# Kernel tuning notes

Measured on AMD Instinct MI355X. Metric: run time of the kernel, lower is better.

## Reference

```python
import jax, jax.numpy as jnp
import numpy as np

D_MODEL = 1024
H = 16
D_K = D_MODEL // H
NEG = -1.0e9


def setup_inputs() -> dict:
    key = jax.random.key(0)
    ks = jax.random.split(key, 12)
    B, S = 2, 2048
    s = 1.0 / np.sqrt(D_MODEL)
    inp = {
        "q": jax.random.normal(ks[0], (B, S, D_MODEL), jnp.float32),
        "k": jax.random.normal(ks[1], (B, S, D_MODEL), jnp.float32),
        "v": jax.random.normal(ks[2], (B, S, D_MODEL), jnp.float32),
        "mask": jnp.tril(jnp.ones((S, S), jnp.int32))[None, None, :, :],
        "wq": jax.random.normal(ks[3], (D_MODEL, D_MODEL), jnp.float32) * s,
        "bq": jax.random.normal(ks[4], (D_MODEL,), jnp.float32) * s,
        "wk": jax.random.normal(ks[5], (D_MODEL, D_MODEL), jnp.float32) * s,
        "bk": jax.random.normal(ks[6], (D_MODEL,), jnp.float32) * s,
        "wv": jax.random.normal(ks[7], (D_MODEL, D_MODEL), jnp.float32) * s,
        "bv": jax.random.normal(ks[8], (D_MODEL,), jnp.float32) * s,
        "wo": jax.random.normal(ks[9], (D_MODEL, D_MODEL), jnp.float32) * s,
        "bo": jax.random.normal(ks[10], (D_MODEL,), jnp.float32) * s,
    }
    return inp


def _split_heads(x):
    # [B,S,D] -> [B,H,S,d_k]
    B, S, _ = x.shape
    return x.reshape(B, S, H, D_K).transpose(0, 2, 1, 3)


def reference(q, k, v, mask, wq, bq, wk, bk, wv, bv, wo, bo):
    # torch Linear: y = x @ W.T + b
    query = _split_heads(q @ wq.T + bq)
    key = _split_heads(k @ wk.T + bk)
    value = _split_heads(v @ wv.T + bv)
    # scores: [B,H,S,S]
    scores = jnp.einsum("bhqd,bhkd->bhqk", query, key) / jnp.sqrt(
        jnp.asarray(D_K, query.dtype))
    scores = jnp.where(mask == 0, jnp.asarray(NEG, scores.dtype), scores)
    attn = jax.nn.softmax(scores, axis=-1)  # dropout p=0.0 -> identity
    x = jnp.einsum("bhqk,bhkd->bhqd", attn, value)
    B, _, S, _ = x.shape
    x = x.transpose(0, 2, 1, 3).reshape(B, S, D_MODEL)
    return x @ wo.T + bo
```

## Files before the change

kernel.cpp:

```cpp
#include <hip/hip_runtime.h>
#include <hip/hip_bf16.h>
#include <cstdint>
#include <cstddef>

#define BATCH 2
#define SEQ   2048
#define DM    1024
#define NH    16
#define DK    64
#define MROWS (BATCH*SEQ)

typedef __bf16 bf16;
typedef float  f32x4  __attribute__((ext_vector_type(4)));
typedef bf16   bf16x8 __attribute__((ext_vector_type(8)));
typedef bf16   bf16x4 __attribute__((ext_vector_type(4)));

#define MFMA32(a, b, c) __builtin_amdgcn_mfma_f32_16x16x32_bf16(a, b, c, 0, 0, 0)

__device__ __forceinline__ void llds16(const void* gc, void* l) {
    void* g = (void*)gc;
    __builtin_amdgcn_global_load_lds(
        (__attribute__((address_space(1))) uint32_t*)g,
        (__attribute__((address_space(3))) uint32_t*)l,
        16, 0, 0);
}

__global__ __launch_bounds__(256) void k_convert(
    const float* __restrict__ q, const float* __restrict__ k, const float* __restrict__ v,
    const float* __restrict__ wq, const float* __restrict__ wk, const float* __restrict__ wv,
    const float* __restrict__ wo,
    bf16* __restrict__ qb, bf16* __restrict__ kb, bf16* __restrict__ vb,
    bf16* __restrict__ wqb, bf16* __restrict__ wkb, bf16* __restrict__ wvb,
    bf16* __restrict__ wob) {
    long t = (long)blockIdx.x * blockDim.x + threadIdx.x;
    const long NQ = (long)MROWS * DM / 4;
    const long NW = (long)DM * DM / 4;
    const float* src; bf16* dst; long off;
    if (t < NQ)            { src = q;  dst = qb;  off = t; }
    else if (t < 2*NQ)     { src = k;  dst = kb;  off = t - NQ; }
    else if (t < 3*NQ)     { src = v;  dst = vb;  off = t - 2*NQ; }
    else {
        long u = t - 3*NQ;
        if (u < NW)        { src = wq; dst = wqb; off = u; }
        else if (u < 2*NW) { src = wk; dst = wkb; off = u - NW; }
        else if (u < 3*NW) { src = wv; dst = wvb; off = u - 2*NW; }
        else               { src = wo; dst = wob; off = u - 3*NW; }
    }
    f32x4 x = *(const f32x4*)(src + off * 4);
    bf16x4 y;
    y[0] = (bf16)x[0]; y[1] = (bf16)x[1]; y[2] = (bf16)x[2]; y[3] = (bf16)x[3];
    *(bf16x4*)(dst + off * 4) = y;
}

__device__ __forceinline__ void gemm_main(const bf16* __restrict__ A, const bf16* __restrict__ B,
                                          int m0, int n0, f32x4 acc[4][4]) {
    constexpr int K = DM, BK = 64;
    __shared__ bf16 sA[16 * 512];
    __shared__ bf16 sB[16 * 512];
    const int tid = threadIdx.x;
    const int l = tid & 63, w = tid >> 6;
    const int lr = l & 15, lc = l >> 4;
    const int wm = w & 1, wn = w >> 1;

    for (int k0 = 0; k0 < K; k0 += BK) {
#pragma unroll
        for (int i = 0; i < 4; ++i) {
            int e = w * 4 + i;
            int kc = e >> 3, t16 = e & 7;
            const bf16* ga = A + (size_t)(m0 + t16 * 16 + lr) * K + k0 + kc * 32 + lc * 8;
            const bf16* gb = B + (size_t)(n0 + t16 * 16 + lr) * K + k0 + kc * 32 + lc * 8;
            llds16(ga, &sA[e * 512]);
            llds16(gb, &sB[e * 512]);
        }
        __syncthreads();

#pragma unroll
        for (int kk = 0; kk < 2; ++kk) {
            bf16x8 af[4], bfr[4];
#pragma unroll
            for (int mi = 0; mi < 4; ++mi)
                af[mi] = *(const bf16x8*)&sA[(size_t)(kk * 8 + wm * 4 + mi) * 512 + l * 8];
#pragma unroll
            for (int ni = 0; ni < 4; ++ni)
                bfr[ni] = *(const bf16x8*)&sB[(size_t)(kk * 8 + wn * 4 + ni) * 512 + l * 8];
#pragma unroll
            for (int mi = 0; mi < 4; ++mi)
#pragma unroll
                for (int ni = 0; ni < 4; ++ni)
                    acc[mi][ni] = MFMA32(af[mi], bfr[ni], acc[mi][ni]);
        }
        __syncthreads();
    }
}

__global__ __launch_bounds__(256) void k_gemm_qkv(
    const bf16* __restrict__ qb, const bf16* __restrict__ kb, const bf16* __restrict__ vb,
    const bf16* __restrict__ wqb, const bf16* __restrict__ wkb, const bf16* __restrict__ wvb,
    const float* __restrict__ bq, const float* __restrict__ bk, const float* __restrict__ bv,
    bf16* __restrict__ Qf, bf16* __restrict__ Kf, bf16* __restrict__ Vf) {
    const int z = blockIdx.z;
    const bf16* A; const bf16* B; const float* bias;
    int m0, n0;
    if (z == 2) {
        A = vb; B = wvb; bias = bv;
        m0 = blockIdx.x * 128;
        n0 = blockIdx.y * 128;
    } else {
        A = z ? wkb : wqb; B = z ? kb : qb; bias = z ? bk : bq;
        m0 = blockIdx.y * 128;
        n0 = blockIdx.x * 128;
    }
    f32x4 acc[4][4] = {};
    gemm_main(A, B, m0, n0, acc);

    const int tid = threadIdx.x, l = tid & 63, w = tid >> 6;
    const int quad = l >> 4, l15 = l & 15;
    const int wm = w & 1, wn = w >> 1;

    if (z == 2) {
#pragma unroll
        for (int ni = 0; ni < 4; ++ni) {
            int dcol = n0 + wn * 64 + ni * 16 + l15;
            int hh2 = dcol >> 6;
            int dtile = (dcol >> 4) & 3;
            float bias_v = bias[dcol];
#pragma unroll
            for (int mi = 0; mi < 4; ++mi) {
                int srow = m0 + wm * 64 + mi * 16;
                int bb = srow >> 11, sl = srow & 2047;
                int kc = sl >> 5;
                int qp = 2 * (mi & 1) + (quad >> 1);
                bf16x4 pack;
#pragma unroll
                for (int r = 0; r < 4; ++r)
                    pack[r] = (bf16)(acc[mi][ni][r] + bias_v);
                size_t entry = ((size_t)(bb * NH + hh2) * 64 + kc) * 4 + dtile;
                *(bf16x4*)(Vf + entry * 512 + (size_t)(qp * 16 + l15) * 8 + (quad & 1) * 4) = pack;
            }
        }
    } else {
        bf16* out = z ? Kf : Qf;
        const float scale = z ? 1.0f : 0.18033688f;
        float bias_rv[4][4];
#pragma unroll
        for (int mi = 0; mi < 4; ++mi)
#pragma unroll
            for (int r = 0; r < 4; ++r)
                bias_rv[mi][r] = bias[m0 + wm * 64 + mi * 16 + quad * 4 + r];
#pragma unroll
        for (int ni = 0; ni < 4; ++ni) {
            int scol = n0 + wn * 64 + ni * 16 + l15;
            int bb = scol >> 11, s = scol & 2047;
            int s16 = s >> 4;
#pragma unroll
            for (int mi = 0; mi < 4; ++mi) {
                int drow = m0 + wm * 64 + mi * 16;
                int hh2 = (drow >> 6) & 15;
                int chunk = (drow & 63) >> 5;
                int qp = 2 * (mi & 1) + (quad >> 1);
                bf16x4 pack;
#pragma unroll
                for (int r = 0; r < 4; ++r)
                    pack[r] = (bf16)((acc[mi][ni][r] + bias_rv[mi][r]) * scale);
                size_t entry = ((size_t)(bb * NH + hh2) * 128 + s16) * 2 + chunk;
                *(bf16x4*)(out + entry * 512 + (size_t)(qp * 16 + l15) * 8 + (quad & 1) * 4) = pack;
            }
        }
    }
}

__global__ __launch_bounds__(256) void k_gemm_out(
    const bf16* __restrict__ X, const bf16* __restrict__ wob,
    const float* __restrict__ bo, float* __restrict__ out) {
    constexpr int K = DM, BK = 64;
    const int m0 = blockIdx.y * 128, n0 = blockIdx.x * 64;
    __shared__ bf16 sA[16 * 512];
    __shared__ bf16 sB[8 * 512];
    const int tid = threadIdx.x;
    const int l = tid & 63, w = tid >> 6;
    const int lr = l & 15, lc = l >> 4;
    const int quad = l >> 4, l15 = l & 15;
    const int wm = w & 1, wn = w >> 1;

    f32x4 acc[4][2] = {};
    for (int k0 = 0; k0 < K; k0 += BK) {
#pragma unroll
        for (int i = 0; i < 4; ++i) {
            int e = w * 4 + i;
            int kc = e >> 3, mt = e & 7;
            llds16(X + (size_t)(m0 + mt * 16 + lr) * K + k0 + kc * 32 + lc * 8, &sA[e * 512]);
        }
#pragma unroll
        for (int i = 0; i < 2; ++i) {
            int e = w * 2 + i;
            int kc = e >> 2, nt = e & 3;
            llds16(wob + (size_t)(n0 + nt * 16 + lr) * K + k0 + kc * 32 + lc * 8, &sB[e * 512]);
        }
        __syncthreads();

#pragma unroll
        for (int kk = 0; kk < 2; ++kk) {
            bf16x8 af[4], bfr[2];
#pragma unroll
            for (int mi = 0; mi < 4; ++mi)
                af[mi] = *(const bf16x8*)&sA[(size_t)(kk * 8 + wm * 4 + mi) * 512 + l * 8];
#pragma unroll
            for (int ni = 0; ni < 2; ++ni)
                bfr[ni] = *(const bf16x8*)&sB[(size_t)(kk * 4 + wn * 2 + ni) * 512 + l * 8];
#pragma unroll
            for (int mi = 0; mi < 4; ++mi)
#pragma unroll
                for (int ni = 0; ni < 2; ++ni)
                    acc[mi][ni] = MFMA32(af[mi], bfr[ni], acc[mi][ni]);
        }
        __syncthreads();
    }
#pragma unroll
    for (int mi = 0; mi < 4; ++mi)
#pragma unroll
        for (int ni = 0; ni < 2; ++ni) {
            int col = n0 + wn * 32 + ni * 16 + l15;
            float bias_v = bo[col];
            int rbase = m0 + wm * 64 + mi * 16 + quad * 4;
#pragma unroll
            for (int r = 0; r < 4; ++r)
                out[(size_t)(rbase + r) * DM + col] = acc[mi][ni][r] + bias_v;
        }
}

__global__ __launch_bounds__(256, 4) void k_flash(const bf16* __restrict__ Qf,
                                                  const bf16* __restrict__ Kf,
                                                  const bf16* __restrict__ Vf,
                                                  bf16* __restrict__ X) {
    const int bh = blockIdx.x;
    const int qt = 31 - (int)blockIdx.y;
    const int b = bh >> 4, h = bh & 15;
    const int tid = threadIdx.x, w = tid >> 6, l = tid & 63;
    const int quad = l >> 4, l15 = l & 15;
    __shared__ bf16 sK[8 * 512];
    __shared__ bf16 sV[8 * 512];
    __shared__ bf16 P[4][16 * 72];
    bf16* Pw = P[w];

    const bf16* qfp = Qf + (size_t)bh * 128 * 1024;
    const bf16* kfp = Kf + (size_t)bh * 128 * 1024;
    const bf16* vfp = Vf + (size_t)bh * 64 * 4 * 512;

    const int qt16 = qt * 4 + w;
    const int qglob = qt16 * 16 + l15;

    bf16x8 qf[2];
#pragma unroll
    for (int c = 0; c < 2; ++c)
        qf[c] = *(const bf16x8*)(qfp + ((size_t)qt16 * 2 + c) * 512 + (size_t)l * 8);

    f32x4 o[4] = {};
    float lp = 0.f;

    for (int j = 0; j <= qt; ++j) {
#pragma unroll
        for (int i = 0; i < 2; ++i) {
            int e = w * 2 + i;
            llds16(kfp + ((size_t)(j * 8 + e)) * 512 + (size_t)l * 8, &sK[e * 512]);
            llds16(vfp + ((size_t)(j * 8 + e)) * 512 + (size_t)l * 8, &sV[e * 512]);
        }
        __syncthreads();

        f32x4 st[4];
#pragma unroll
        for (int ni = 0; ni < 4; ++ni) {
            bf16x8 k0 = *(const bf16x8*)&sK[(size_t)(ni * 2 + 0) * 512 + l * 8];
            bf16x8 k1 = *(const bf16x8*)&sK[(size_t)(ni * 2 + 1) * 512 + l * 8];
            f32x4 zz = {};
            zz = MFMA32(k0, qf[0], zz);
            st[ni] = MFMA32(k1, qf[1], zz);
        }

        const bool diag = (j == qt);
#pragma unroll
        for (int ni = 0; ni < 4; ++ni) {
            bf16x4 ev;
#pragma unroll
            for (int r = 0; r < 4; ++r) {
                float s = st[ni][r];
                if (diag) {
                    int key = j * 64 + ni * 16 + quad * 4 + r;
                    if (key > qglob) s = -1e30f;
                }
                float e = __builtin_amdgcn_exp2f(s);
                lp += e;
                ev[r] = (bf16)e;
            }
            *(bf16x4*)&Pw[l15 * 72 + ni * 16 + quad * 4] = ev;
        }

#pragma unroll
        for (int c = 0; c < 2; ++c) {
            bf16x8 pb = *(const bf16x8*)&Pw[l15 * 72 + c * 32 + quad * 8];
#pragma unroll
            for (int dt = 0; dt < 4; ++dt) {
                bf16x8 vv = *(const bf16x8*)&sV[(size_t)(c * 4 + dt) * 512 + l * 8];
                o[dt] = MFMA32(vv, pb, o[dt]);
            }
        }
        __syncthreads();
    }

    lp += __shfl_xor(lp, 16, 64);
    lp += __shfl_xor(lp, 32, 64);
    float rv = 1.f / lp;

#pragma unroll
    for (int dt = 0; dt < 4; ++dt) {
        bf16x4 pk;
#pragma unroll
        for (int r = 0; r < 4; ++r)
            pk[r] = (bf16)(o[dt][r] * rv);
        *(bf16x4*)&Pw[l15 * 72 + dt * 16 + quad * 4] = pk;
    }
#pragma unroll
    for (int i = 0; i < 2; ++i) {
        int row = i * 8 + (l >> 3);
        bf16x8 vv = *(const bf16x8*)&Pw[row * 72 + (l & 7) * 8];
        *(bf16x8*)(X + (size_t)(b * SEQ + qt16 * 16 + row) * DM + h * 64 + (l & 7) * 8) = vv;
    }
}

extern "C" void kernel_launch(void* const* d_in, const int* in_sizes, int n_in,
                              void* d_out, int out_size, void* d_ws, size_t ws_size,
                              hipStream_t stream) {
    const float* q  = (const float*)d_in[0];
    const float* k  = (const float*)d_in[1];
    const float* v  = (const float*)d_in[2];
    const float* wq = (const float*)d_in[4];
    const float* bq = (const float*)d_in[5];
    const float* wk = (const float*)d_in[6];
    const float* bk = (const float*)d_in[7];
    const float* wv = (const float*)d_in[8];
    const float* bv = (const float*)d_in[9];
    const float* wo = (const float*)d_in[10];
    const float* bo = (const float*)d_in[11];
    float* out = (float*)d_out;

    uint8_t* ws = (uint8_t*)d_ws;
    const size_t SZ_ACT = (size_t)MROWS * DM * sizeof(bf16);
    const size_t SZ_W   = (size_t)DM * DM * sizeof(bf16);
    bf16* qb  = (bf16*)(ws);
    bf16* kb  = (bf16*)(ws + SZ_ACT);
    bf16* vb  = (bf16*)(ws + 2 * SZ_ACT);
    bf16* wqb = (bf16*)(ws + 3 * SZ_ACT);
    bf16* wkb = (bf16*)(ws + 3 * SZ_ACT + SZ_W);
    bf16* wvb = (bf16*)(ws + 3 * SZ_ACT + 2 * SZ_W);
    bf16* wob = (bf16*)(ws + 3 * SZ_ACT + 3 * SZ_W);
    bf16* Qf  = (bf16*)(ws + 3 * SZ_ACT + 4 * SZ_W);
    bf16* Kf  = (bf16*)(ws + 4 * SZ_ACT + 4 * SZ_W);
    bf16* Vf  = (bf16*)(ws + 5 * SZ_ACT + 4 * SZ_W);
    bf16* X   = (bf16*)(ws + 6 * SZ_ACT + 4 * SZ_W);

    {
        long total_vec4 = 3L * MROWS * DM / 4 + 4L * DM * DM / 4;
        k_convert<<<dim3((unsigned)(total_vec4 / 256)), 256, 0, stream>>>(
            q, k, v, wq, wk, wv, wo, qb, kb, vb, wqb, wkb, wvb, wob);
    }
    k_gemm_qkv<<<dim3(32, 8, 3), 256, 0, stream>>>(
        qb, kb, vb, wqb, wkb, wvb, bq, bk, bv, Qf, Kf, Vf);
    k_flash<<<dim3(BATCH * NH, SEQ / 64), 256, 0, stream>>>(Qf, Kf, Vf, X);
    k_gemm_out<<<dim3(DM / 64, MROWS / 128), 256, 0, stream>>>(X, wob, bo, out);
}
```

Before: 250.6 us.

## Double-buffer K/V tiles in flash attention and shrink GEMM K-step

The flash kernel now keeps K and V in one LDS area with two buffers. It prefetches the next key block's K/V with direct global-to-LDS loads while the current block is computed, and drops the trailing barrier so there is one sync per iteration. This is meant to hide global load latency behind the MFMA and softmax work. The extra LDS lowers the occupancy hint from 4 to 3 blocks. Separately, both projection GEMMs halve their K-step to 32, which cuts shared memory use but doubles the number of barrier-separated load/compute rounds.

```diff
diff --git a/kernel.cpp b/kernel.cpp
--- a/kernel.cpp
+++ b/kernel.cpp
@@ -54,9 +54,9 @@
 
 __device__ __forceinline__ void gemm_main(const bf16* __restrict__ A, const bf16* __restrict__ B,
                                           int m0, int n0, f32x4 acc[4][4]) {
-    constexpr int K = DM, BK = 64;
-    __shared__ bf16 sA[16 * 512];
-    __shared__ bf16 sB[16 * 512];
+    constexpr int K = DM, BK = 32;
+    __shared__ bf16 sA[8 * 512];
+    __shared__ bf16 sB[8 * 512];
     const int tid = threadIdx.x;
     const int l = tid & 63, w = tid >> 6;
     const int lr = l & 15, lc = l >> 4;
@@ -64,31 +64,27 @@
 
     for (int k0 = 0; k0 < K; k0 += BK) {
 #pragma unroll
-        for (int i = 0; i < 4; ++i) {
-            int e = w * 4 + i;
-            int kc = e >> 3, t16 = e & 7;
-            const bf16* ga = A + (size_t)(m0 + t16 * 16 + lr) * K + k0 + kc * 32 + lc * 8;
-            const bf16* gb = B + (size_t)(n0 + t16 * 16 + lr) * K + k0 + kc * 32 + lc * 8;
+        for (int i = 0; i < 2; ++i) {
+            int e = w * 2 + i;
+            const bf16* ga = A + (size_t)(m0 + e * 16 + lr) * K + k0 + lc * 8;
+            const bf16* gb = B + (size_t)(n0 + e * 16 + lr) * K + k0 + lc * 8;
             llds16(ga, &sA[e * 512]);
             llds16(gb, &sB[e * 512]);
         }
         __syncthreads();
 
-#pragma unroll
-        for (int kk = 0; kk < 2; ++kk) {
-            bf16x8 af[4], bfr[4];
-#pragma unroll
-            for (int mi = 0; mi < 4; ++mi)
-                af[mi] = *(const bf16x8*)&sA[(size_t)(kk * 8 + wm * 4 + mi) * 512 + l * 8];
+        bf16x8 af[4], bfr[4];
+#pragma unroll
+        for (int mi = 0; mi < 4; ++mi)
+            af[mi] = *(const bf16x8*)&sA[(size_t)(wm * 4 + mi) * 512 + l * 8];
+#pragma unroll
+        for (int ni = 0; ni < 4; ++ni)
+            bfr[ni] = *(const bf16x8*)&sB[(size_t)(wn * 4 + ni) * 512 + l * 8];
+#pragma unroll
+        for (int mi = 0; mi < 4; ++mi)
 #pragma unroll
             for (int ni = 0; ni < 4; ++ni)
-                bfr[ni] = *(const bf16x8*)&sB[(size_t)(kk * 8 + wn * 4 + ni) * 512 + l * 8];
-#pragma unroll
-            for (int mi = 0; mi < 4; ++mi)
-#pragma unroll
-                for (int ni = 0; ni < 4; ++ni)
-                    acc[mi][ni] = MFMA32(af[mi], bfr[ni], acc[mi][ni]);
-        }
+                acc[mi][ni] = MFMA32(af[mi], bfr[ni], acc[mi][ni]);
         __syncthreads();
     }
 }
@@ -172,10 +168,10 @@
 __global__ __launch_bounds__(256) void k_gemm_out(
     const bf16* __restrict__ X, const bf16* __restrict__ wob,
     const float* __restrict__ bo, float* __restrict__ out) {
-    constexpr int K = DM, BK = 64;
+    constexpr int K = DM, BK = 32;
     const int m0 = blockIdx.y * 128, n0 = blockIdx.x * 64;
-    __shared__ bf16 sA[16 * 512];
-    __shared__ bf16 sB[8 * 512];
+    __shared__ bf16 sA[8 * 512];
+    __shared__ bf16 sB[4 * 512];
     const int tid = threadIdx.x;
     const int l = tid & 63, w = tid >> 6;
     const int lr = l & 15, lc = l >> 4;
@@ -185,34 +181,25 @@
     f32x4 acc[4][2] = {};
     for (int k0 = 0; k0 < K; k0 += BK) {
 #pragma unroll
-        for (int i = 0; i < 4; ++i) {
-            int e = w * 4 + i;
-            int kc = e >> 3, mt = e & 7;
-            llds16(X + (size_t)(m0 + mt * 16 + lr) * K + k0 + kc * 32 + lc * 8, &sA[e * 512]);
-        }
-#pragma unroll
         for (int i = 0; i < 2; ++i) {
             int e = w * 2 + i;
-            int kc = e >> 2, nt = e & 3;
-            llds16(wob + (size_t)(n0 + nt * 16 + lr) * K + k0 + kc * 32 + lc * 8, &sB[e * 512]);
-        }
-        __syncthreads();
-
-#pragma unroll
-        for (int kk = 0; kk < 2; ++kk) {
-            bf16x8 af[4], bfr[2];
-#pragma unroll
-            for (int mi = 0; mi < 4; ++mi)
-                af[mi] = *(const bf16x8*)&sA[(size_t)(kk * 8 + wm * 4 + mi) * 512 + l * 8];
+            llds16(X + (size_t)(m0 + e * 16 + lr) * K + k0 + lc * 8, &sA[e * 512]);
+        }
+        llds16(wob + (size_t)(n0 + w * 16 + lr) * K + k0 + lc * 8, &sB[w * 512]);
+        __syncthreads();
+
+        bf16x8 af[4], bfr[2];
+#pragma unroll
+        for (int mi = 0; mi < 4; ++mi)
+            af[mi] = *(const bf16x8*)&sA[(size_t)(wm * 4 + mi) * 512 + l * 8];
+#pragma unroll
+        for (int ni = 0; ni < 2; ++ni)
+            bfr[ni] = *(const bf16x8*)&sB[(size_t)(wn * 2 + ni) * 512 + l * 8];
+#pragma unroll
+        for (int mi = 0; mi < 4; ++mi)
 #pragma unroll
             for (int ni = 0; ni < 2; ++ni)
-                bfr[ni] = *(const bf16x8*)&sB[(size_t)(kk * 4 + wn * 2 + ni) * 512 + l * 8];
-#pragma unroll
-            for (int mi = 0; mi < 4; ++mi)
-#pragma unroll
-                for (int ni = 0; ni < 2; ++ni)
-                    acc[mi][ni] = MFMA32(af[mi], bfr[ni], acc[mi][ni]);
-        }
+                acc[mi][ni] = MFMA32(af[mi], bfr[ni], acc[mi][ni]);
         __syncthreads();
     }
 #pragma unroll
@@ -228,7 +215,7 @@
         }
 }
 
-__global__ __launch_bounds__(256, 4) void k_flash(const bf16* __restrict__ Qf,
+__global__ __launch_bounds__(256, 3) void k_flash(const bf16* __restrict__ Qf,
                                                   const bf16* __restrict__ Kf,
                                                   const bf16* __restrict__ Vf,
                                                   bf16* __restrict__ X) {
@@ -237,8 +224,7 @@
     const int b = bh >> 4, h = bh & 15;
     const int tid = threadIdx.x, w = tid >> 6, l = tid & 63;
     const int quad = l >> 4, l15 = l & 15;
-    __shared__ bf16 sK[8 * 512];
-    __shared__ bf16 sV[8 * 512];
+    __shared__ bf16 sKV[2][16 * 512];
     __shared__ bf16 P[4][16 * 72];
     bf16* Pw = P[w];
 
@@ -257,20 +243,33 @@
     f32x4 o[4] = {};
     float lp = 0.f;
 
+#pragma unroll
+    for (int i = 0; i < 4; ++i) {
+        int e = w * 4 + i;
+        const bf16* src = (e < 8) ? kfp + ((size_t)(0 * 8 + e)) * 512
+                                  : vfp + ((size_t)(0 * 8 + (e - 8))) * 512;
+        llds16(src + (size_t)l * 8, &sKV[0][e * 512]);
+    }
+
     for (int j = 0; j <= qt; ++j) {
-#pragma unroll
-        for (int i = 0; i < 2; ++i) {
-            int e = w * 2 + i;
-            llds16(kfp + ((size_t)(j * 8 + e)) * 512 + (size_t)l * 8, &sK[e * 512]);
-            llds16(vfp + ((size_t)(j * 8 + e)) * 512 + (size_t)l * 8, &sV[e * 512]);
-        }
-        __syncthreads();
+        __syncthreads();
+        const bf16* cur = sKV[j & 1];
+        if (j < qt) {
+            int j1 = j + 1;
+#pragma unroll
+            for (int i = 0; i < 4; ++i) {
+                int e = w * 4 + i;
+                const bf16* src = (e < 8) ? kfp + ((size_t)(j1 * 8 + e)) * 512
+                                          : vfp + ((size_t)(j1 * 8 + (e - 8))) * 512;
+                llds16(src + (size_t)l * 8, (void*)&sKV[j1 & 1][e * 512]);
+            }
+        }
 
         f32x4 st[4];
 #pragma unroll
         for (int ni = 0; ni < 4; ++ni) {
-            bf16x8 k0 = *(const bf16x8*)&sK[(size_t)(ni * 2 + 0) * 512 + l * 8];
-            bf16x8 k1 = *(const bf16x8*)&sK[(size_t)(ni * 2 + 1) * 512 + l * 8];
+            bf16x8 k0 = *(const bf16x8*)&cur[(size_t)(ni * 2 + 0) * 512 + l * 8];
+            bf16x8 k1 = *(const bf16x8*)&cur[(size_t)(ni * 2 + 1) * 512 + l * 8];
             f32x4 zz = {};
             zz = MFMA32(k0, qf[0], zz);
             st[ni] = MFMA32(k1, qf[1], zz);
@@ -299,11 +298,10 @@
             bf16x8 pb = *(const bf16x8*)&Pw[l15 * 72 + c * 32 + quad * 8];
 #pragma unroll
             for (int dt = 0; dt < 4; ++dt) {
-                bf16x8 vv = *(const bf16x8*)&sV[(size_t)(c * 4 + dt) * 512 + l * 8];
+                bf16x8 vv = *(const bf16x8*)&cur[(size_t)(8 + c * 4 + dt) * 512 + l * 8];
                 o[dt] = MFMA32(vv, pb, o[dt]);
             }
         }
-        __syncthreads();
     }
 
     lp += __shfl_xor(lp, 16, 64);
```

New measurement: 252.2 us. Within noise of the previous version (+0.6%).
